# Kernel optimization log

Measured on AMD Instinct MI355X. Metric: run time of the kernel, lower is better.

The kernel has to match this reference:

```python
import jax, jax.numpy as jnp
import numpy as np

B, T, D = 64, 32, 256
NFC = 2 * D          # num_inputs_fc = 512
DIMS = [4 * D, NFC, NFC // 2, NFC // 4, NFC // 8, 4]  # last layer padded to 4 outs
H = 4                # camera, rot, trans, plane heads stacked


def setup_inputs() -> dict:
    key = jax.random.key(0)
    ks = jax.random.split(key, 12)
    inp = {
        "emb": jax.random.normal(ks[0], (B, T, D), dtype=jnp.float32),
        # each of n0, n1 in [1,16] so n0+n1 <= T=32 and no divide-by-zero
        "num_planes": jax.random.randint(ks[1], (B, 2), 1, 17, dtype=jnp.int32),
    }
    for i in range(5):
        fan_in = DIMS[i]
        scale = 1.0 / np.sqrt(fan_in)
        inp[f"w{i}"] = jax.random.uniform(ks[2 + 2 * i], (H, DIMS[i], DIMS[i + 1]),
                                           minval=-scale, maxval=scale, dtype=jnp.float32)
        inp[f"b{i}"] = jax.random.uniform(ks[3 + 2 * i], (H, DIMS[i + 1]),
                                           minval=-scale, maxval=scale, dtype=jnp.float32)
    return inp


def _forward(emb, num_planes, w0, b0, w1, b1, w2, b2, w3, b3, w4, b4):
    Bs, Ts, Ds = emb.shape
    n0 = num_planes[:, 0]
    n1 = num_planes[:, 1]
    idx = jnp.arange(Ts)
    # img1 global feature: mean of tokens t < n0 (original zeroes t>=n0 then sums / n0)
    m1 = (idx[None, :] < n0[:, None])                                  # (B,T) bool
    g1 = (emb * m1[..., None].astype(emb.dtype)).sum(1) / n0[:, None].astype(emb.dtype)
    # img2 global feature: mean of tokens n0 <= t < n0+n1
    in2 = (idx[None, :] >= n0[:, None]) & (idx[None, :] < (n0 + n1)[:, None])  # (B,T)
    g2 = (emb * in2[..., None].astype(emb.dtype)).sum(1) / n1[:, None].astype(emb.dtype)
    # pairwise concat: [emb_i, emb_j, g1, g2] -> (B,T,T,4D)
    ei = jnp.broadcast_to(emb[:, :, None, :], (Bs, Ts, Ts, Ds))
    ej = jnp.broadcast_to(emb[:, None, :, :], (Bs, Ts, Ts, Ds))
    g1b = jnp.broadcast_to(g1[:, None, None, :], (Bs, Ts, Ts, Ds))
    g2b = jnp.broadcast_to(g2[:, None, None, :], (Bs, Ts, Ts, Ds))
    cat = jnp.concatenate([ei, ej, g1b, g2b], axis=-1)
    # 4 stacked MLP heads (camera, rot, trans, plane); final layer padded to 4 outputs
    h = jax.nn.relu(jnp.einsum('btsd,hdk->hbtsk', cat, w0) + b0[:, None, None, None, :])
    h = jax.nn.relu(jnp.einsum('hbtsd,hdk->hbtsk', h, w1) + b1[:, None, None, None, :])
    h = jax.nn.relu(jnp.einsum('hbtsd,hdk->hbtsk', h, w2) + b2[:, None, None, None, :])
    h = jax.nn.relu(jnp.einsum('hbtsd,hdk->hbtsk', h, w3) + b3[:, None, None, None, :])
    h = jnp.einsum('hbtsd,hdk->hbtsk', h, w4) + b4[:, None, None, None, :]  # (4,B,T,T,4)
    camera = h[0, ..., 0]            # (B,T,T)
    rot = h[1]                       # (B,T,T,4)
    trans = h[2, ..., :3]            # (B,T,T,3)
    plane_corr = jax.nn.sigmoid(h[3, ..., 0])  # (B,T,T)
    # valid pairs: row i < n0, col j in [n0, n0+n1)  (== ~padding_mask)
    valid = m1[:, :, None] & in2[:, None, :]                           # (B,T,T) bool
    v = valid.astype(emb.dtype)
    pf = (n0 * n1).astype(emb.dtype)
    camera_corr = jax.nn.sigmoid((camera * v).sum((1, 2)) / pf)        # (B,)
    rot_res = (rot * v[..., None]).sum((1, 2)) / pf[:, None]           # (B,4)
    trans_res = (trans * v[..., None]).sum((1, 2)) / pf[:, None]       # (B,3)
    return camera_corr, rot_res, trans_res, plane_corr, valid


def reference(emb, num_planes, w0, b0, w1, b1, w2, b2, w3, b3, w4, b4):
    return _forward(emb, num_planes, w0, b0, w1, b1, w2, b2, w3, b3, w4, b4)
```

## Files before the change

kernel.cpp:

```cpp
#include <hip/hip_runtime.h>

typedef float f32x4 __attribute__((ext_vector_type(4)));
typedef short short8 __attribute__((ext_vector_type(8)));
typedef unsigned short ushort_t;
typedef unsigned int uint_t;

constexpr int O_CAM   = 0;
constexpr int O_ROT   = 64;
constexpr int O_TRANS = 320;
constexpr int O_PLANE = 512;
constexpr int O_VALID = 66048;

constexpr size_t B_G1   = 0;
constexpr size_t B_G2   = 65536;
constexpr size_t B_ACC  = 131072;
constexpr size_t B_ABF  = 133120;
constexpr size_t B_CBF  = 8521728;
constexpr size_t B_BT1  = 16910336;
constexpr size_t B_BT2  = 17958912;
constexpr size_t B_BT3  = 18221056;
constexpr size_t B_BT0F = 18286592;
constexpr size_t B_BT4  = 22480896;

__device__ __forceinline__ ushort_t f2bf(float f) {
    uint_t u = __float_as_uint(f);
    return (ushort_t)((u + 0x7FFFu + ((u >> 16) & 1u)) >> 16);
}

__device__ __forceinline__ uint_t cvt_pk_bf16(float lo, float hi) {
    uint_t r;
    asm("v_cvt_pk_bf16_f32 %0, %1, %2" : "=v"(r) : "v"(lo), "v"(hi));
    return r;
}

__device__ __forceinline__ uint_t bfadd2_relu(uint_t a, uint_t c) {
    const float lo = __uint_as_float(a << 16) + __uint_as_float(c << 16);
    const float hi = __uint_as_float(a & 0xffff0000u) + __uint_as_float(c & 0xffff0000u);
    return cvt_pk_bf16(fmaxf(lo, 0.f), fmaxf(hi, 0.f));
}

__global__ __launch_bounds__(256) void k_prepA(
    const float* __restrict__ emb, const int* __restrict__ np_,
    const float* __restrict__ w0, ushort_t* __restrict__ bt0f,
    float* __restrict__ g1, float* __restrict__ g2)
{
    __shared__ float stg[4][32][18];
    const int l = threadIdx.x & 63;
    const int u = threadIdx.x >> 6;
    const int c = blockIdx.x * 4 + u;
    if (c >= 4160) return;
    if (c < 4096) {
        const int h = c >> 10, ks = (c >> 5) & 31, nt = c & 31;
        const float* src = w0 + ((size_t)h*1024 + ks*32 + (l >> 1))*512 + nt*16 + (l & 1)*8;
        const float4 v0 = *(const float4*)(src);
        const float4 v1 = *(const float4*)(src + 4);
        float* srow = &stg[u][l >> 1][(l & 1)*8];
        srow[0]=v0.x; srow[1]=v0.y; srow[2]=v0.z; srow[3]=v0.w;
        srow[4]=v1.x; srow[5]=v1.y; srow[6]=v1.z; srow[7]=v1.w;
        asm volatile("s_waitcnt lgkmcnt(0)" ::: "memory");
        const int d0 = (l >> 4) << 3, n = l & 15;
        short8 o;
        #pragma unroll
        for (int j = 0; j < 8; ++j) o[j] = (short)f2bf(stg[u][d0 + j][n]);
        *(short8*)(bt0f + (size_t)c*512 + (size_t)l*8) = o;
    } else {
        const int b = c - 4096;
        const int n0 = np_[2*b], n1 = np_[2*b+1];
        const float* e = emb + (size_t)b*8192;
        #pragma unroll
        for (int dd = 0; dd < 4; ++dd) {
            const int d = l + 64*dd;
            float a1 = 0.f, a2 = 0.f;
            for (int t = 0; t < 32; ++t) {
                float v = e[t*256 + d];
                if (t < n0) a1 += v;
                else if (t < n0 + n1) a2 += v;
            }
            g1[b*256 + d] = a1 / n0;
            g2[b*256 + d] = a2 / n1;
        }
    }
}

__global__ __launch_bounds__(256) void k_ACp(
    const float* __restrict__ emb, const ushort_t* __restrict__ bt0f,
    const float* __restrict__ g1, const float* __restrict__ g2,
    const float* __restrict__ b0,
    ushort_t* __restrict__ Abf, ushort_t* __restrict__ Cbf,
    const float* __restrict__ w1, const float* __restrict__ w2, const float* __restrict__ w3,
    const float* __restrict__ w4,
    ushort_t* __restrict__ bt1, ushort_t* __restrict__ bt2, ushort_t* __restrict__ bt3,
    ushort_t* __restrict__ bt4,
    const int* __restrict__ np_, float* __restrict__ accz, float* __restrict__ out)
{
    __shared__ __align__(16) char es[16384];
    __shared__ __align__(16) ushort_t gs[512];
    __shared__ float stg[4][32][18];

    const int tid = threadIdx.x;
    const int l = tid & 63;

    if (blockIdx.x >= 512) {
        const int u = tid >> 6;
        int c = (blockIdx.x - 512) * 4 + u;
        if (c >= 1417) return;
        if (c < 1344) {
            const float* w; ushort_t* dst; int K, N;
            if (c < 1024)      {           w = w1; dst = bt1 + (size_t)c*512; K = 512; N = 256; }
            else if (c < 1280) { c -= 1024; w = w2; dst = bt2 + (size_t)c*512; K = 256; N = 128; }
            else               { c -= 1280; w = w3; dst = bt3 + (size_t)c*512; K = 128; N = 64;  }
            const int NT = N/16, KS_NT = (K/32)*NT;
            const int h = c / KS_NT, rem = c % KS_NT, ks = rem / NT, nt = rem % NT;
            const float* src = w + ((size_t)h*K + ks*32 + (l >> 1))*N + nt*16 + (l & 1)*8;
            const float4 v0 = *(const float4*)(src);
            const float4 v1 = *(const float4*)(src + 4);
            float* srow = &stg[u][l >> 1][(l & 1)*8];
            srow[0]=v0.x; srow[1]=v0.y; srow[2]=v0.z; srow[3]=v0.w;
            srow[4]=v1.x; srow[5]=v1.y; srow[6]=v1.z; srow[7]=v1.w;
            asm volatile("s_waitcnt lgkmcnt(0)" ::: "memory");
            const int d0 = (l >> 4) << 3, n = l & 15;
            short8 o;
            #pragma unroll
            for (int j = 0; j < 8; ++j) o[j] = (short)f2bf(stg[u][d0 + j][n]);
            *(short8*)(dst + (size_t)l*8) = o;
        } else if (c == 1344) {
            #pragma unroll
            for (int i = 0; i < 8; ++i) accz[l*8 + i] = 0.f;
        } else if (c < 1409) {
            const int b = c - 1345;
            const int n0 = np_[2*b], n1 = np_[2*b+1];
            float* dst = out + O_VALID + b*1024;
            #pragma unroll
            for (int i = 0; i < 16; ++i) {
                const int j = l*16 + i;
                const int t = j >> 5, s = j & 31;
                dst[j] = (t < n0 && s >= n0 && s < n0 + n1) ? 1.f : 0.f;
            }
        } else {
            const int uu = c - 1409;
            const int h = uu >> 1, ks = uu & 1;
            const int n = l & 15;
            const int d0 = ks*32 + ((l >> 4) << 3);
            short8 o;
            #pragma unroll
            for (int j = 0; j < 8; ++j)
                o[j] = (n < 4) ? (short)f2bf(w4[(size_t)h*256 + (d0 + j)*4 + n]) : (short)0;
            *(short8*)(bt4 + ((size_t)uu*64 + l)*8) = o;
        }
        return;
    }

    const int b = blockIdx.x & 63, hc = blockIdx.x >> 6;
    const int h = hc >> 1, isC = hc & 1;
    const int w4w = tid >> 6;
    const int lrow = l & 15, lko = l >> 4;

    {
        const float* eb = emb + (size_t)b*8192;
        #pragma unroll
        for (int j = 0; j < 16; ++j) {
            const int flat = j*256 + tid;
            const int row = flat >> 7, cp = flat & 127;
            const float2 v = *(const float2*)(eb + row*256 + cp*2);
            const uint_t p = (uint_t)f2bf(v.x) | ((uint_t)f2bf(v.y) << 16);
            const int byte = (row*512 + cp*4) ^ ((row & 7) << 4);
            *(uint_t*)(es + byte) = p;
        }
    }
    if (!isC && tid < 64) {
        const float* src = (tid < 32) ? (g1 + b*256 + tid*8) : (g2 + b*256 + (tid - 32)*8);
        const float4 v0 = *(const float4*)(src);
        const float4 v1 = *(const float4*)(src + 4);
        short8 o;
        o[0] = (short)f2bf(v0.x); o[1] = (short)f2bf(v0.y);
        o[2] = (short)f2bf(v0.z); o[3] = (short)f2bf(v0.w);
        o[4] = (short)f2bf(v1.x); o[5] = (short)f2bf(v1.y);
        o[6] = (short)f2bf(v1.z); o[7] = (short)f2bf(v1.w);
        *(short8*)(gs + tid*8) = o;
    }
    __syncthreads();

    f32x4 acc[2][8];
    #pragma unroll
    for (int mt = 0; mt < 2; ++mt)
        #pragma unroll
        for (int nt = 0; nt < 8; ++nt) acc[mt][nt] = (f32x4){0.f,0.f,0.f,0.f};

    const ushort_t* basef = bt0f + (size_t)h*(32*32*512) + (size_t)(w4w*8)*512 + (size_t)l*8;

    {
        const int ksE0 = isC ? 8 : 0;
        for (int kk = 0; kk < 8; ++kk) {
            short8 bfv[8];
            const ushort_t* bp = basef + (size_t)(ksE0 + kk)*16384;
            #pragma unroll
            for (int nt = 0; nt < 8; ++nt) bfv[nt] = *(const short8*)(bp + nt*512);
            const int o = (lrow*512 + kk*64 + lko*16) ^ ((lrow & 7) << 4);
            const short8 a0 = *(const short8*)(es + o);
            const short8 a1 = *(const short8*)(es + o + 8192);
            __builtin_amdgcn_s_setprio(1);
            #pragma unroll
            for (int nt = 0; nt < 8; ++nt) {
                acc[0][nt] = __builtin_amdgcn_mfma_f32_16x16x32_bf16(a0, bfv[nt], acc[0][nt], 0, 0, 0);
                acc[1][nt] = __builtin_amdgcn_mfma_f32_16x16x32_bf16(a1, bfv[nt], acc[1][nt], 0, 0, 0);
            }
            __builtin_amdgcn_s_setprio(0);
        }
    }
    if (!isC) {
        for (int kk = 0; kk < 16; ++kk) {
            short8 bfv[8];
            const ushort_t* bp = basef + (size_t)(16 + kk)*16384;
            #pragma unroll
            for (int nt = 0; nt < 8; ++nt) bfv[nt] = *(const short8*)(bp + nt*512);
            const short8 ag = *(const short8*)(gs + kk*32 + lko*8);
            __builtin_amdgcn_s_setprio(1);
            #pragma unroll
            for (int nt = 0; nt < 8; ++nt) {
                acc[0][nt] = __builtin_amdgcn_mfma_f32_16x16x32_bf16(ag, bfv[nt], acc[0][nt], 0, 0, 0);
                acc[1][nt] = __builtin_amdgcn_mfma_f32_16x16x32_bf16(ag, bfv[nt], acc[1][nt], 0, 0, 0);
            }
            __builtin_amdgcn_s_setprio(0);
        }
    }

    ushort_t* dst = (isC ? Cbf : Abf) + (size_t)(h*64 + b)*32*512;
    #pragma unroll
    for (int nt = 0; nt < 8; ++nt) {
        const int col = (w4w*8 + nt)*16 + lrow;
        const float g = isC ? 0.f : b0[h*512 + col];
        #pragma unroll
        for (int mt = 0; mt < 2; ++mt)
            #pragma unroll
            for (int r = 0; r < 4; ++r) {
                const int row = mt*16 + lko*4 + r;
                dst[row*512 + col] = f2bf(acc[mt][nt][r] + g);
            }
    }
}

__global__ __launch_bounds__(512, 2) void k_mlp(
    const ushort_t* __restrict__ Abf, const ushort_t* __restrict__ Cbf,
    const ushort_t* __restrict__ bt1, const ushort_t* __restrict__ bt2,
    const ushort_t* __restrict__ bt3, const ushort_t* __restrict__ bt4,
    const float* __restrict__ b1, const float* __restrict__ b2, const float* __restrict__ b3,
    const float* __restrict__ b4,
    const int* __restrict__ np_, float* __restrict__ out, float* __restrict__ accbuf)
{
    const int x = blockIdx.x;
    const bool isH3 = (x < 1024);
    int h, b, t0;
    int n0 = 0, n1 = 0;
    if (isH3) {
        h = 3; b = x >> 4; t0 = (x & 15) * 2;
    } else {
        const int y = x - 1024;
        h = y >> 8; b = (y >> 2) & 63; t0 = (y & 3) * 4;
        n0 = np_[2*b]; n1 = np_[2*b+1];
        if (t0 >= n0) return;
    }

    __shared__ __align__(16) char smem[65536];
    char* X   = smem;
    char* X2  = smem + 49152;
    char* X3b = smem + 32768;

    const int tid = threadIdx.x;
    const int l = tid & 63, w = tid >> 6;
    const int lrow = l & 15, lko = l >> 4;
    const size_t hb = (size_t)(h*64 + b);
    const uint4* Arows = (const uint4*)(Abf + hb*32*512);
    const uint4* Crows = (const uint4*)(Cbf + hb*32*512);

    const float bias1_0 = b1[h*256 + (w*2 + 0)*16 + lrow];
    const float bias1_1 = b1[h*256 + (w*2 + 1)*16 + lrow];
    const float bias2v  = b2[h*128 + w*16 + lrow];
    const float bias3v  = b3[h*64 + (w & 3)*16 + lrow];
    const float bias4v  = b4[h*4 + (lrow & 3)];

    const ushort_t* bp1 = bt1 + (size_t)(h*256 + w*2)*512 + (size_t)l*8;
    short8 bb[2][2];
    bb[0][0] = *(const short8*)(bp1);
    bb[0][1] = *(const short8*)(bp1 + 512);

    #pragma unroll
    for (int i = 0; i < 8; ++i) {
        const int flat = i*512 + tid;
        const int row = flat >> 6, q4 = flat & 63;
        int trow, crow;
        if (isH3) { trow = t0 + (row >> 5); crow = row & 31; }
        else      { trow = t0 + (row >> 4); crow = n0 + (row & 15); }
        const uint4 aa = Arows[(size_t)trow*64 + q4];
        const uint4 cc = Crows[(size_t)crow*64 + q4];
        uint4 v;
        v.x = bfadd2_relu(aa.x, cc.x);
        v.y = bfadd2_relu(aa.y, cc.y);
        v.z = bfadd2_relu(aa.z, cc.z);
        v.w = bfadd2_relu(aa.w, cc.w);
        *(uint4*)(X + ((row*1024 + q4*16) ^ ((row & 7) << 4))) = v;
    }
    __syncthreads();

    f32x4 acc1[4][2];
    #pragma unroll
    for (int mt = 0; mt < 4; ++mt) {
        acc1[mt][0] = (f32x4){bias1_0, bias1_0, bias1_0, bias1_0};
        acc1[mt][1] = (f32x4){bias1_1, bias1_1, bias1_1, bias1_1};
    }

    #pragma unroll
    for (int ks = 0; ks < 16; ++ks) {
        if (ks < 15) {
            bb[(ks+1)&1][0] = *(const short8*)(bp1 + (size_t)(ks+1)*8192);
            bb[(ks+1)&1][1] = *(const short8*)(bp1 + (size_t)(ks+1)*8192 + 512);
        }
        const short8 bf0 = bb[ks&1][0];
        const short8 bf1 = bb[ks&1][1];
        __builtin_amdgcn_s_setprio(1);
        #pragma unroll
        for (int mt = 0; mt < 4; ++mt) {
            const short8 a0 = *(const short8*)(X + (((mt*16 + lrow)*1024 + ks*64 + lko*16) ^ ((lrow & 7) << 4)));
            acc1[mt][0] = __builtin_amdgcn_mfma_f32_16x16x32_bf16(a0, bf0, acc1[mt][0], 0, 0, 0);
            acc1[mt][1] = __builtin_amdgcn_mfma_f32_16x16x32_bf16(a0, bf1, acc1[mt][1], 0, 0, 0);
        }
        __builtin_amdgcn_s_setprio(0);
    }
    __syncthreads();

    #pragma unroll
    for (int nt = 0; nt < 2; ++nt) {
        const int col = (w*2 + nt)*16 + lrow;
        #pragma unroll
        for (int mt = 0; mt < 4; ++mt)
            #pragma unroll
            for (int r = 0; r < 4; ++r) {
                const int row = mt*16 + lko*4 + r;
                const float v = fmaxf(acc1[mt][nt][r], 0.f);
                *(ushort_t*)(X + ((row*512 + col*2) ^ ((row & 7) << 4))) =
                    (ushort_t)cvt_pk_bf16(v, v);
            }
    }
    __syncthreads();

    f32x4 acc2[4];
    #pragma unroll
    for (int mt = 0; mt < 4; ++mt) acc2[mt] = (f32x4){bias2v, bias2v, bias2v, bias2v};
    {
        const ushort_t* bp = bt2 + (size_t)(h*64 + w)*512 + (size_t)l*8;
        short8 b2b[2];
        b2b[0] = *(const short8*)(bp);
        #pragma unroll
        for (int ks = 0; ks < 8; ++ks) {
            if (ks < 7) b2b[(ks+1)&1] = *(const short8*)(bp + (size_t)(ks+1)*4096);
            __builtin_amdgcn_s_setprio(1);
            #pragma unroll
            for (int mt = 0; mt < 4; ++mt) {
                const short8 a0 = *(const short8*)(X + (((mt*16 + lrow)*512 + ks*64 + lko*16) ^ ((lrow & 7) << 4)));
                acc2[mt] = __builtin_amdgcn_mfma_f32_16x16x32_bf16(a0, b2b[ks&1], acc2[mt], 0, 0, 0);
            }
            __builtin_amdgcn_s_setprio(0);
        }
    }
    {
        const int col = w*16 + lrow;
        #pragma unroll
        for (int mt = 0; mt < 4; ++mt)
            #pragma unroll
            for (int r = 0; r < 4; ++r) {
                const int row = mt*16 + lko*4 + r;
                const float v = fmaxf(acc2[mt][r], 0.f);
                *(ushort_t*)(X2 + ((row*256 + col*2) ^ ((row & 7) << 4))) =
                    (ushort_t)cvt_pk_bf16(v, v);
            }
    }
    __syncthreads();

    const int mhalf = w >> 2;
    f32x4 acc3[2];
    acc3[0] = (f32x4){bias3v, bias3v, bias3v, bias3v};
    acc3[1] = (f32x4){bias3v, bias3v, bias3v, bias3v};
    {
        const ushort_t* bp = bt3 + (size_t)(h*16 + (w & 3))*512 + (size_t)l*8;
        #pragma unroll
        for (int ks = 0; ks < 4; ++ks) {
            const short8 bf = *(const short8*)(bp + (size_t)ks*2048);
            __builtin_amdgcn_s_setprio(1);
            #pragma unroll
            for (int mi = 0; mi < 2; ++mi) {
                const int mt = mhalf*2 + mi;
                const short8 a0 = *(const short8*)(X2 + (((mt*16 + lrow)*256 + ks*64 + lko*16) ^ ((lrow & 7) << 4)));
                acc3[mi] = __builtin_amdgcn_mfma_f32_16x16x32_bf16(a0, bf, acc3[mi], 0, 0, 0);
            }
            __builtin_amdgcn_s_setprio(0);
        }
    }
    {
        const int col = (w & 3)*16 + lrow;
        #pragma unroll
        for (int mi = 0; mi < 2; ++mi) {
            const int mt = mhalf*2 + mi;
            #pragma unroll
            for (int r = 0; r < 4; ++r) {
                const int row = mt*16 + lko*4 + r;
                const float v = fmaxf(acc3[mi][r], 0.f);
                *(ushort_t*)(X3b + ((row*128 + col*2) ^ ((row & 7) << 4))) =
                    (ushort_t)cvt_pk_bf16(v, v);
            }
        }
    }
    __syncthreads();

    if (w < 4) {
        const int mt = w;
        f32x4 acc4 = (f32x4){bias4v, bias4v, bias4v, bias4v};
        const ushort_t* bp = bt4 + (size_t)(h*2)*512 + (size_t)l*8;
        #pragma unroll
        for (int ks = 0; ks < 2; ++ks) {
            const short8 bf = *(const short8*)(bp + (size_t)ks*512);
            const short8 a0 = *(const short8*)(X3b + (((mt*16 + lrow)*128 + ks*64 + lko*16) ^ ((lrow & 7) << 4)));
            acc4 = __builtin_amdgcn_mfma_f32_16x16x32_bf16(a0, bf, acc4, 0, 0, 0);
        }

        if (isH3) {
            if (lrow == 0) {
                #pragma unroll
                for (int r = 0; r < 4; ++r) {
                    const int row = mt*16 + lko*4 + r;
                    out[O_PLANE + b*1024 + (t0 + (row >> 5))*32 + (row & 31)] =
                        1.f / (1.f + expf(-acc4[r]));
                }
            }
        } else {
            const int nj = (h == 0) ? 1 : ((h == 1) ? 4 : 3);
            float v = 0.f;
            #pragma unroll
            for (int r = 0; r < 4; ++r) {
                const int row = mt*16 + lko*4 + r;
                const int tq = row >> 4, sr = row & 15;
                if ((t0 + tq) < n0 && sr < n1) v += acc4[r];
            }
            v += __shfl_down(v, 32);
            v += __shfl_down(v, 16);
            if (lko == 0 && lrow < nj) {
                const int slot = (h == 0) ? 0 : ((h == 1) ? 1 + lrow : 5 + lrow);
                atomicAdd(&accbuf[b*8 + slot], v);
            }
        }
    }
}

__global__ __launch_bounds__(512) void k_final(
    const int* __restrict__ np_, const float* __restrict__ acc, float* __restrict__ out)
{
    const int tid = threadIdx.x;
    const int b = tid >> 3, sl = tid & 7;
    const int n0 = np_[2*b], n1 = np_[2*b+1];
    const float pf = (float)(n0 * n1);
    const float v = acc[b*8 + sl] / pf;
    if (sl == 0)      out[O_CAM + b] = 1.f / (1.f + expf(-v));
    else if (sl <= 4) out[O_ROT + b*4 + (sl - 1)] = v;
    else              out[O_TRANS + b*3 + (sl - 5)] = v;
}

extern "C" void kernel_launch(void* const* d_in, const int* in_sizes, int n_in,
                              void* d_out, int out_size, void* d_ws, size_t ws_size,
                              hipStream_t stream) {
    (void)in_sizes; (void)n_in; (void)out_size; (void)ws_size;
    const float* emb = (const float*)d_in[0];
    const int*   np_ = (const int*)d_in[1];
    const float* w0  = (const float*)d_in[2];
    const float* b0  = (const float*)d_in[3];
    const float* w1  = (const float*)d_in[4];
    const float* b1  = (const float*)d_in[5];
    const float* w2  = (const float*)d_in[6];
    const float* b2  = (const float*)d_in[7];
    const float* w3  = (const float*)d_in[8];
    const float* b3  = (const float*)d_in[9];
    const float* w4  = (const float*)d_in[10];
    const float* b4  = (const float*)d_in[11];

    char* W = (char*)d_ws;
    float* out = (float*)d_out;
    float*    g1   = (float*)(W + B_G1);
    float*    g2   = (float*)(W + B_G2);
    float*    acc  = (float*)(W + B_ACC);
    ushort_t* Abf  = (ushort_t*)(W + B_ABF);
    ushort_t* Cbf  = (ushort_t*)(W + B_CBF);
    ushort_t* bt1  = (ushort_t*)(W + B_BT1);
    ushort_t* bt2  = (ushort_t*)(W + B_BT2);
    ushort_t* bt3  = (ushort_t*)(W + B_BT3);
    ushort_t* bt0f = (ushort_t*)(W + B_BT0F);
    ushort_t* bt4  = (ushort_t*)(W + B_BT4);

    k_prepA<<<1040, 256, 0, stream>>>(emb, np_, w0, bt0f, g1, g2);
    k_ACp<<<867, 256, 0, stream>>>(emb, bt0f, g1, g2, b0, Abf, Cbf,
                                   w1, w2, w3, w4, bt1, bt2, bt3, bt4, np_, acc, out);
    k_mlp<<<1792, 512, 0, stream>>>(Abf, Cbf, bt1, bt2, bt3, bt4,
                                    b1, b2, b3, b4, np_, out, acc);
    k_final<<<1, 512, 0, stream>>>(np_, acc, out);
}
```

Before: 84.95 us.

## Switch MLP layers 1-2 to 32x32x16 bf16 MFMA with matching weight pre-layout

Layers 1 and 2 of the per-pair MLP now use 32x32x16 bf16 MFMA tiles instead of 16x16x32. Each wave computes a 32-wide column block over 32-row tiles, with the accumulator row mapping and LDS XOR swizzles changed to match. The weight repacking prologue emits a 32-column, 16-K tile layout for w1/w2 through a padded staging buffer. The larger MFMA should cut LDS A-fragment reads per FLOP and the instruction count, at the cost of more accumulator registers and new swizzle patterns that could cause bank conflicts or correctness issues.

```diff
diff --git a/kernel.cpp b/kernel.cpp
--- a/kernel.cpp
+++ b/kernel.cpp
@@ -1,6 +1,7 @@
 #include <hip/hip_runtime.h>
 
 typedef float f32x4 __attribute__((ext_vector_type(4)));
+typedef float f32x16 __attribute__((ext_vector_type(16)));
 typedef short short8 __attribute__((ext_vector_type(8)));
 typedef unsigned short ushort_t;
 typedef unsigned int uint_t;
@@ -104,25 +105,44 @@
         const int u = tid >> 6;
         int c = (blockIdx.x - 512) * 4 + u;
         if (c >= 1417) return;
-        if (c < 1344) {
-            const float* w; ushort_t* dst; int K, N;
-            if (c < 1024)      {           w = w1; dst = bt1 + (size_t)c*512; K = 512; N = 256; }
-            else if (c < 1280) { c -= 1024; w = w2; dst = bt2 + (size_t)c*512; K = 256; N = 128; }
-            else               { c -= 1280; w = w3; dst = bt3 + (size_t)c*512; K = 128; N = 64;  }
-            const int NT = N/16, KS_NT = (K/32)*NT;
-            const int h = c / KS_NT, rem = c % KS_NT, ks = rem / NT, nt = rem % NT;
-            const float* src = w + ((size_t)h*K + ks*32 + (l >> 1))*N + nt*16 + (l & 1)*8;
+        float* F = &stg[u][0][0];
+        if (c < 1280) {
+            const float* w; ushort_t* dst; int K, N, h, ks, nt;
+            if (c < 1024) {
+                h = c >> 8; const int rem = c & 255; ks = rem >> 3; nt = rem & 7;
+                w = w1; K = 512; N = 256; dst = bt1 + (size_t)c*512;
+            } else {
+                const int c2 = c - 1024;
+                h = c2 >> 6; const int rem = c2 & 63; ks = rem >> 2; nt = rem & 3;
+                w = w2; K = 256; N = 128; dst = bt2 + (size_t)c2*512;
+            }
+            const float* src = w + ((size_t)(h*K + ks*16 + (l >> 2)))*N + nt*32 + (l & 3)*8;
             const float4 v0 = *(const float4*)(src);
             const float4 v1 = *(const float4*)(src + 4);
-            float* srow = &stg[u][l >> 1][(l & 1)*8];
+            float* srow = F + (l >> 2)*33 + (l & 3)*8;
             srow[0]=v0.x; srow[1]=v0.y; srow[2]=v0.z; srow[3]=v0.w;
             srow[4]=v1.x; srow[5]=v1.y; srow[6]=v1.z; srow[7]=v1.w;
             asm volatile("s_waitcnt lgkmcnt(0)" ::: "memory");
-            const int d0 = (l >> 4) << 3, n = l & 15;
             short8 o;
             #pragma unroll
-            for (int j = 0; j < 8; ++j) o[j] = (short)f2bf(stg[u][d0 + j][n]);
+            for (int j = 0; j < 8; ++j)
+                o[j] = (short)f2bf(F[((l >> 5)*8 + j)*33 + (l & 31)]);
             *(short8*)(dst + (size_t)l*8) = o;
+        } else if (c < 1344) {
+            const int c3 = c - 1280;
+            const int h = c3 >> 4, rem = c3 & 15, ks = rem >> 2, nt = rem & 3;
+            const float* src = w3 + ((size_t)(h*128 + ks*32 + (l >> 1)))*64 + nt*16 + (l & 1)*8;
+            const float4 v0 = *(const float4*)(src);
+            const float4 v1 = *(const float4*)(src + 4);
+            float* srow = F + (l >> 1)*18 + (l & 1)*8;
+            srow[0]=v0.x; srow[1]=v0.y; srow[2]=v0.z; srow[3]=v0.w;
+            srow[4]=v1.x; srow[5]=v1.y; srow[6]=v1.z; srow[7]=v1.w;
+            asm volatile("s_waitcnt lgkmcnt(0)" ::: "memory");
+            short8 o;
+            #pragma unroll
+            for (int j = 0; j < 8; ++j)
+                o[j] = (short)f2bf(F[(((l >> 4) << 3) + j)*18 + (l & 15)]);
+            *(short8*)(bt3 + (size_t)c3*512 + (size_t)l*8) = o;
         } else if (c == 1344) {
             #pragma unroll
             for (int i = 0; i < 8; ++i) accz[l*8 + i] = 0.f;
@@ -268,20 +288,19 @@
     const int tid = threadIdx.x;
     const int l = tid & 63, w = tid >> 6;
     const int lrow = l & 15, lko = l >> 4;
+    const int l31 = l & 31, lh16 = (l >> 5) * 16;
     const size_t hb = (size_t)(h*64 + b);
     const uint4* Arows = (const uint4*)(Abf + hb*32*512);
     const uint4* Crows = (const uint4*)(Cbf + hb*32*512);
 
-    const float bias1_0 = b1[h*256 + (w*2 + 0)*16 + lrow];
-    const float bias1_1 = b1[h*256 + (w*2 + 1)*16 + lrow];
-    const float bias2v  = b2[h*128 + w*16 + lrow];
-    const float bias3v  = b3[h*64 + (w & 3)*16 + lrow];
-    const float bias4v  = b4[h*4 + (lrow & 3)];
-
-    const ushort_t* bp1 = bt1 + (size_t)(h*256 + w*2)*512 + (size_t)l*8;
-    short8 bb[2][2];
-    bb[0][0] = *(const short8*)(bp1);
-    bb[0][1] = *(const short8*)(bp1 + 512);
+    const float bias1v = b1[h*256 + w*32 + l31];
+    const float bias2v = b2[h*128 + (w & 3)*32 + l31];
+    const float bias3v = b3[h*64 + (w & 3)*16 + lrow];
+    const float bias4v = b4[h*4 + (lrow & 3)];
+
+    const ushort_t* bp1 = bt1 + (size_t)(h*256 + w)*512 + (size_t)l*8;
+    short8 bb[2];
+    bb[0] = *(const short8*)(bp1);
 
     #pragma unroll
     for (int i = 0; i < 8; ++i) {
@@ -297,81 +316,73 @@
         v.y = bfadd2_relu(aa.y, cc.y);
         v.z = bfadd2_relu(aa.z, cc.z);
         v.w = bfadd2_relu(aa.w, cc.w);
-        *(uint4*)(X + ((row*1024 + q4*16) ^ ((row & 7) << 4))) = v;
+        *(uint4*)(X + ((row*1024 + q4*16) ^ ((row & 31) << 4))) = v;
     }
     __syncthreads();
 
-    f32x4 acc1[4][2];
+    f32x16 acc1[2];
     #pragma unroll
-    for (int mt = 0; mt < 4; ++mt) {
-        acc1[mt][0] = (f32x4){bias1_0, bias1_0, bias1_0, bias1_0};
-        acc1[mt][1] = (f32x4){bias1_1, bias1_1, bias1_1, bias1_1};
-    }
-
+    for (int i = 0; i < 16; ++i) { acc1[0][i] = bias1v; acc1[1][i] = bias1v; }
+
+    const int xbase0 = l31*1024;
+    const int xrA = l31 << 4;
     #pragma unroll
-    for (int ks = 0; ks < 16; ++ks) {
-        if (ks < 15) {
-            bb[(ks+1)&1][0] = *(const short8*)(bp1 + (size_t)(ks+1)*8192);
-            bb[(ks+1)&1][1] = *(const short8*)(bp1 + (size_t)(ks+1)*8192 + 512);
-        }
-        const short8 bf0 = bb[ks&1][0];
-        const short8 bf1 = bb[ks&1][1];
+    for (int ks = 0; ks < 32; ++ks) {
+        if (ks < 31) bb[(ks+1) & 1] = *(const short8*)(bp1 + (size_t)(ks+1)*4096);
+        const int off = (ks*32 + lh16) ^ xrA;
         __builtin_amdgcn_s_setprio(1);
-        #pragma unroll
-        for (int mt = 0; mt < 4; ++mt) {
-            const short8 a0 = *(const short8*)(X + (((mt*16 + lrow)*1024 + ks*64 + lko*16) ^ ((lrow & 7) << 4)));
-            acc1[mt][0] = __builtin_amdgcn_mfma_f32_16x16x32_bf16(a0, bf0, acc1[mt][0], 0, 0, 0);
-            acc1[mt][1] = __builtin_amdgcn_mfma_f32_16x16x32_bf16(a0, bf1, acc1[mt][1], 0, 0, 0);
-        }
+        const short8 a0 = *(const short8*)(X + xbase0 + off);
+        acc1[0] = __builtin_amdgcn_mfma_f32_32x32x16_bf16(a0, bb[ks & 1], acc1[0], 0, 0, 0);
+        const short8 a1 = *(const short8*)(X + xbase0 + 32768 + off);
+        acc1[1] = __builtin_amdgcn_mfma_f32_32x32x16_bf16(a1, bb[ks & 1], acc1[1], 0, 0, 0);
         __builtin_amdgcn_s_setprio(0);
     }
     __syncthreads();
 
+    {
+        const int colX1x2 = (w*32 + l31) * 2;
+        #pragma unroll
+        for (int mt = 0; mt < 2; ++mt)
+            #pragma unroll
+            for (int r = 0; r < 16; ++r) {
+                const int row = mt*32 + (r & 3) + 8*(r >> 2) + 4*(l >> 5);
+                const float v = fmaxf(acc1[mt][r], 0.f);
+                *(ushort_t*)(X + ((row*512 + colX1x2) ^ ((row & 15) << 4))) =
+                    (ushort_t)cvt_pk_bf16(v, v);
+            }
+    }
+    __syncthreads();
+
+    f32x16 acc2;
     #pragma unroll
-    for (int nt = 0; nt < 2; ++nt) {
-        const int col = (w*2 + nt)*16 + lrow;
-        #pragma unroll
-        for (int mt = 0; mt < 4; ++mt)
-            #pragma unroll
-            for (int r = 0; r < 4; ++r) {
-                const int row = mt*16 + lko*4 + r;
-                const float v = fmaxf(acc1[mt][nt][r], 0.f);
-                *(ushort_t*)(X + ((row*512 + col*2) ^ ((row & 7) << 4))) =
-                    (ushort_t)cvt_pk_bf16(v, v);
-            }
-    }
-    __syncthreads();
-
-    f32x4 acc2[4];
-    #pragma unroll
-    for (int mt = 0; mt < 4; ++mt) acc2[mt] = (f32x4){bias2v, bias2v, bias2v, bias2v};
-    {
-        const ushort_t* bp = bt2 + (size_t)(h*64 + w)*512 + (size_t)l*8;
+    for (int i = 0; i < 16; ++i) acc2[i] = bias2v;
+    {
+        const int mt2 = w >> 2;
+        const ushort_t* bp2 = bt2 + (size_t)(h*64 + (w & 3))*512 + (size_t)l*8;
+        const int xbase2 = (mt2*32 + l31) * 512;
+        const int xrB = lrow << 4;
         short8 b2b[2];
-        b2b[0] = *(const short8*)(bp);
-        #pragma unroll
-        for (int ks = 0; ks < 8; ++ks) {
-            if (ks < 7) b2b[(ks+1)&1] = *(const short8*)(bp + (size_t)(ks+1)*4096);
+        b2b[0] = *(const short8*)(bp2);
+        #pragma unroll
+        for (int ks = 0; ks < 16; ++ks) {
+            if (ks < 15) b2b[(ks+1) & 1] = *(const short8*)(bp2 + (size_t)(ks+1)*2048);
+            const int off = (ks*32 + lh16) ^ xrB;
             __builtin_amdgcn_s_setprio(1);
-            #pragma unroll
-            for (int mt = 0; mt < 4; ++mt) {
-                const short8 a0 = *(const short8*)(X + (((mt*16 + lrow)*512 + ks*64 + lko*16) ^ ((lrow & 7) << 4)));
-                acc2[mt] = __builtin_amdgcn_mfma_f32_16x16x32_bf16(a0, b2b[ks&1], acc2[mt], 0, 0, 0);
-            }
+            const short8 a0 = *(const short8*)(X + xbase2 + off);
+            acc2 = __builtin_amdgcn_mfma_f32_32x32x16_bf16(a0, b2b[ks & 1], acc2, 0, 0, 0);
             __builtin_amdgcn_s_setprio(0);
         }
     }
     {
-        const int col = w*16 + lrow;
-        #pragma unroll
-        for (int mt = 0; mt < 4; ++mt)
-            #pragma unroll
-            for (int r = 0; r < 4; ++r) {
-                const int row = mt*16 + lko*4 + r;
-                const float v = fmaxf(acc2[mt][r], 0.f);
-                *(ushort_t*)(X2 + ((row*256 + col*2) ^ ((row & 7) << 4))) =
-                    (ushort_t)cvt_pk_bf16(v, v);
-            }
+        const int colX2x2 = ((w & 3)*32 + l31) * 2;
+        const int mt2 = w >> 2;
+        #pragma unroll
+        for (int r = 0; r < 16; ++r) {
+            const int row = mt2*32 + (r & 3) + 8*(r >> 2) + 4*(l >> 5);
+            const float v = fmaxf(acc2[r], 0.f);
+            *(ushort_t*)(X2 + ((row*256 + colX2x2) ^ ((row & 15) << 4))) =
+                (ushort_t)cvt_pk_bf16(v, v);
+        }
     }
     __syncthreads();
 
@@ -388,7 +399,8 @@
             #pragma unroll
             for (int mi = 0; mi < 2; ++mi) {
                 const int mt = mhalf*2 + mi;
-                const short8 a0 = *(const short8*)(X2 + (((mt*16 + lrow)*256 + ks*64 + lko*16) ^ ((lrow & 7) << 4)));
+                const int row = mt*16 + lrow;
+                const short8 a0 = *(const short8*)(X2 + ((row*256 + ks*64 + lko*16) ^ ((row & 15) << 4)));
                 acc3[mi] = __builtin_amdgcn_mfma_f32_16x16x32_bf16(a0, bf, acc3[mi], 0, 0, 0);
             }
             __builtin_amdgcn_s_setprio(0);
```

Measured after the change: 92.55 us. 1.09x slower.
